# Kernel tuning notes

Measured on AMD Instinct MI355X. Metric: run time of the kernel, lower is better.

The kernel has to match this reference:

```python
import jax, jax.numpy as jnp
import numpy as np

EPS = 1e-8
N_ITERS = 5
B, L, K = 8192, 512, 4
EXP_SMOOTH = 0.99


def setup_inputs() -> dict:
    key = jax.random.key(0)
    k1, k2 = jax.random.split(key)
    windows = jax.random.normal(k1, (B, L), dtype=jnp.float32)
    noise = jax.random.normal(k2, (B, K), dtype=jnp.float32)  # replaces torch.randn_like
    init_centers = jnp.linspace(-0.75, 0.75, K, dtype=jnp.float32)
    init_scales = jnp.ones((K,), jnp.float32)
    init_weights = jnp.ones((K,), jnp.float32) / K
    prior_w_param = jnp.ones((1,), jnp.float32) * 10.0
    # log(exp_smooth ** arange(L-1, -1, -1)) reshaped to [L, 1]
    log_weights = (jnp.arange(L - 1, -1, -1, dtype=jnp.float32) * np.float32(np.log(EXP_SMOOTH))).reshape(L, 1)
    blend_param = jnp.ones((1,), jnp.float32) * 10.0
    return dict(windows=windows, noise=noise, init_centers=init_centers,
                init_scales=init_scales, init_weights=init_weights,
                prior_w_param=prior_w_param, log_weights=log_weights,
                blend_param=blend_param)


def _forward(windows, noise, init_centers, init_scales, init_weights,
             prior_w_param, log_weights, blend_param):
    # ---- _initialize_parameters ----
    data_mean = jnp.mean(windows, axis=-1, keepdims=True)        # [B,1]
    data_std = jnp.std(windows, axis=-1, ddof=1, keepdims=True)  # [B,1] (torch unbiased std)
    mu = init_centers[None, :] * data_std + data_mean            # [B,K]
    mu = mu + noise * data_std * 0.01                            # additive init noise
    sigma = jnp.abs(init_scales)[None, :] * data_std             # [B,K]
    w = jnp.broadcast_to(init_weights[None, :], mu.shape)        # [B,K]
    w, mu, sigma = w[:, None, :], mu[:, None, :], sigma[:, None, :]  # [B,1,K]

    # ---- _get_parameters ----
    weights = jnp.exp(log_weights)             # [L,1] exp-smoothing window weights
    blender = jax.nn.sigmoid(blend_param)      # [1]
    prior_w = jax.nn.sigmoid(prior_w_param)    # [1]

    x = windows[..., None]                     # [B,L,1]
    # NOTE: faithful to source — the loop never feeds (p,a,b) back into (w,mu,sigma),
    # so every iteration computes the identical E/M step.
    for _ in range(N_ITERS):
        # E-step: responsibilities via stable logsumexp over components
        log_mix = -0.5 * ((x - mu) / (sigma + EPS)) ** 2 + jnp.log((w + EPS) / (sigma + EPS))  # [B,L,K]
        g = jnp.exp(log_mix - jax.scipy.special.logsumexp(log_mix, axis=-1, keepdims=True))    # [B,L,K]
        # M-step
        wg = g * weights                                                  # [B,L,K]
        sum_g = jnp.maximum(jnp.sum(wg, axis=-2, keepdims=True), EPS)     # [B,1,K]
        p = sum_g + prior_w
        p = p / jnp.sum(p, axis=-1, keepdims=True)                        # mixture weights
        data_mu = jnp.sum(wg * x, axis=-2, keepdims=True) / sum_g         # [B,1,K]
        prior_mu = jnp.mean(x, axis=-2, keepdims=True)                    # [B,1,1] (broadcast ~ repeat)
        a = data_mu * blender + prior_mu * (1.0 - blender)                # blended means
        diff = x - a                                                      # [B,L,K]
        prior_var = jnp.var(x, axis=-2, ddof=1, keepdims=True)            # [B,1,1] unbiased
        data_var = jnp.sum(wg * diff ** 2, axis=-2, keepdims=True) / sum_g
        b = jnp.sqrt(data_var * blender + prior_var * (1.0 - blender) + EPS)  # blended stds
    return g, jnp.squeeze(p, -2), jnp.squeeze(a, -2), jnp.squeeze(b, -2)


def reference(windows, noise, init_centers, init_scales, init_weights,
              prior_w_param, log_weights, blend_param):
    return _forward(windows, noise, init_centers, init_scales, init_weights,
                    prior_w_param, log_weights, blend_param)
```

## Files before the change

### kernel.cpp

```cpp
#include <hip/hip_runtime.h>

#define EPS 1e-8f
constexpr int Bn = 8192, Ln = 512, Kn = 4;
constexpr int EPT = Ln / 64;

typedef float f32x4 __attribute__((ext_vector_type(4)));

__global__ __launch_bounds__(256, 4) void em_kernel(
    const float* __restrict__ windows,
    const float* __restrict__ noise,
    const float* __restrict__ init_centers,
    const float* __restrict__ init_scales,
    const float* __restrict__ init_weights,
    const float* __restrict__ prior_w_param,
    const float* __restrict__ log_weights,
    const float* __restrict__ blend_param,
    float* __restrict__ g_out,
    float* __restrict__ p_out,
    float* __restrict__ a_out,
    float* __restrict__ b_out)
{
    const int wave = threadIdx.x >> 6;
    const int lane = threadIdx.x & 63;
    const int gw   = blockIdx.x * 4 + wave;
    const int rowA = gw * 2;
    const int rowB = rowA + 1;

    float xA[EPT], xB[EPT], wl[EPT];
    const float* xrowA = windows + (size_t)rowA * Ln;
    const float* xrowB = windows + (size_t)rowB * Ln;
    #pragma unroll
    for (int j = 0; j < EPT; ++j) xA[j] = xrowA[lane + 64 * j];
    #pragma unroll
    for (int j = 0; j < EPT; ++j) xB[j] = xrowB[lane + 64 * j];
    #pragma unroll
    for (int j = 0; j < EPT; ++j) wl[j] = log_weights[lane + 64 * j];
    float nzA[Kn], nzB[Kn];
    #pragma unroll
    for (int k = 0; k < Kn; ++k) nzA[k] = noise[(size_t)rowA * Kn + k];
    #pragma unroll
    for (int k = 0; k < Kn; ++k) nzB[k] = noise[(size_t)rowB * Kn + k];

    const float pw = 1.0f / (1.0f + __expf(-prior_w_param[0]));
    const float bl = 1.0f / (1.0f + __expf(-blend_param[0]));

    #pragma unroll
    for (int j = 0; j < EPT; ++j) wl[j] = __expf(wl[j]);

    #pragma unroll
    for (int r = 0; r < 2; ++r) {
        const int    row = (r == 0) ? rowA : rowB;
        const float* x   = (r == 0) ? xA   : xB;
        const float* nz  = (r == 0) ? nzA  : nzB;

        float s = 0.f, sq = 0.f;
        #pragma unroll
        for (int j = 0; j < EPT; ++j) { s += x[j]; sq = fmaf(x[j], x[j], sq); }
        #pragma unroll
        for (int off = 32; off; off >>= 1) {
            s  += __shfl_xor(s,  off, 64);
            sq += __shfl_xor(sq, off, 64);
        }
        const float mean = s * (1.0f / (float)Ln);
        float var = (sq - s * s * (1.0f / (float)Ln)) * (1.0f / (float)(Ln - 1));
        var = fmaxf(var, 0.f);
        const float stdv = sqrtf(var);

        float mu[Kn], inv_sig[Kn], logc[Kn];
        #pragma unroll
        for (int k = 0; k < Kn; ++k) {
            float m  = fmaf(init_centers[k], stdv, mean) + nz[k] * stdv * 0.01f;
            float is = 1.0f / (fabsf(init_scales[k]) * stdv + EPS);
            mu[k]      = m;
            inv_sig[k] = is;
            logc[k]    = __logf((init_weights[k] + EPS) * is);
        }

        float s0[Kn] = {0,0,0,0}, s1[Kn] = {0,0,0,0}, s2[Kn] = {0,0,0,0};

        #pragma unroll
        for (int j = 0; j < EPT; ++j) {
            const int   l  = lane + 64 * j;
            const float xv = x[j];
            float lm[Kn];
            float mx = -1e30f;
            #pragma unroll
            for (int k = 0; k < Kn; ++k) {
                float t = (xv - mu[k]) * inv_sig[k];
                lm[k] = fmaf(t * t, -0.5f, logc[k]);
                mx = fmaxf(mx, lm[k]);
            }
            float e[Kn], sum = 0.f;
            #pragma unroll
            for (int k = 0; k < Kn; ++k) { e[k] = __expf(lm[k] - mx); sum += e[k]; }
            float inv = 1.0f / sum;
            f32x4 gv;
            gv.x = e[0] * inv; gv.y = e[1] * inv; gv.z = e[2] * inv; gv.w = e[3] * inv;
            reinterpret_cast<f32x4*>(g_out)[(size_t)row * Ln + l] = gv;

            float c   = wl[j] * inv;
            float xc  = xv * c;
            float x2c = xv * xc;
            #pragma unroll
            for (int k = 0; k < Kn; ++k) {
                s0[k] = fmaf(e[k], c,   s0[k]);
                s1[k] = fmaf(e[k], xc,  s1[k]);
                s2[k] = fmaf(e[k], x2c, s2[k]);
            }
        }

        #pragma unroll
        for (int k = 0; k < Kn; ++k) {
            #pragma unroll
            for (int off = 32; off; off >>= 1) {
                s0[k] += __shfl_xor(s0[k], off, 64);
                s1[k] += __shfl_xor(s1[k], off, 64);
                s2[k] += __shfl_xor(s2[k], off, 64);
            }
        }

        if (lane < Kn) {
            const int k = lane;
            float psum = 0.f;
            #pragma unroll
            for (int kk = 0; kk < Kn; ++kk) psum += fmaxf(s0[kk], EPS) + pw;
            float sg   = fmaxf(s0[k], EPS);
            float dmu  = s1[k] / sg;
            float av   = dmu * bl + mean * (1.0f - bl);
            float dvar = (s2[k] - 2.0f * av * s1[k] + av * av * s0[k]) / sg;
            float bv   = sqrtf(dvar * bl + var * (1.0f - bl) + EPS);
            p_out[(size_t)row * Kn + k] = (sg + pw) / psum;
            a_out[(size_t)row * Kn + k] = av;
            b_out[(size_t)row * Kn + k] = bv;
        }
    }
}

extern "C" void kernel_launch(void* const* d_in, const int* in_sizes, int n_in,
                              void* d_out, int out_size, void* d_ws, size_t ws_size,
                              hipStream_t stream) {
    const float* windows       = (const float*)d_in[0];
    const float* noise         = (const float*)d_in[1];
    const float* init_centers  = (const float*)d_in[2];
    const float* init_scales   = (const float*)d_in[3];
    const float* init_weights  = (const float*)d_in[4];
    const float* prior_w_param = (const float*)d_in[5];
    const float* log_weights   = (const float*)d_in[6];
    const float* blend_param   = (const float*)d_in[7];

    float* out = (float*)d_out;
    const size_t G  = (size_t)Bn * Ln * Kn;
    const size_t BK = (size_t)Bn * Kn;
    float* g_out = out;
    float* p_out = out + G;
    float* a_out = out + G + BK;
    float* b_out = out + G + 2 * BK;

    em_kernel<<<dim3(Bn / 8), dim3(256), 0, stream>>>(
        windows, noise, init_centers, init_scales, init_weights,
        prior_w_param, log_weights, blend_param,
        g_out, p_out, a_out, b_out);
}
```

Baseline: 24.28 us.

## Split EM into separate stats and streaming kernels using workspace

Splits the fused kernel into two kernels. A stats kernel computes per-row mean, variance and the initial component parameters and writes them to a workspace. A streaming kernel then reads those values, reloads the window rows and does the E/M pass with one row per wave instead of two. The aim is to shorten the serial dependency inside each wave and expose more parallelism, at the cost of a second kernel launch, a second read of the windows, and a workspace round-trip. The original fused kernel remains as a fallback when the workspace is too small.

```diff
diff --git a/kernel.cpp b/kernel.cpp
--- a/kernel.cpp
+++ b/kernel.cpp
@@ -3,10 +3,151 @@
 #define EPS 1e-8f
 constexpr int Bn = 8192, Ln = 512, Kn = 4;
 constexpr int EPT = Ln / 64;
+constexpr int WS_STRIDE = 16;
 
 typedef float f32x4 __attribute__((ext_vector_type(4)));
 
-__global__ __launch_bounds__(256, 4) void em_kernel(
+__global__ __launch_bounds__(256, 8) void stats_kernel(
+    const float* __restrict__ windows,
+    const float* __restrict__ noise,
+    const float* __restrict__ init_centers,
+    const float* __restrict__ init_scales,
+    const float* __restrict__ init_weights,
+    float* __restrict__ ws)
+{
+    const int wave = threadIdx.x >> 6;
+    const int lane = threadIdx.x & 63;
+    const int row  = blockIdx.x * 4 + wave;
+
+    const float* xr = windows + (size_t)row * Ln;
+    float x[EPT];
+    #pragma unroll
+    for (int j = 0; j < EPT; ++j) x[j] = xr[lane + 64 * j];
+
+    float s = 0.f, sq = 0.f;
+    #pragma unroll
+    for (int j = 0; j < EPT; ++j) { s += x[j]; sq = fmaf(x[j], x[j], sq); }
+    #pragma unroll
+    for (int off = 32; off; off >>= 1) {
+        s  += __shfl_xor(s,  off, 64);
+        sq += __shfl_xor(sq, off, 64);
+    }
+    const float mean = s * (1.0f / (float)Ln);
+    float var = (sq - s * s * (1.0f / (float)Ln)) * (1.0f / (float)(Ln - 1));
+    var = fmaxf(var, 0.f);
+    const float stdv = sqrtf(var);
+
+    if (lane < Kn) {
+        const int k  = lane;
+        float m  = fmaf(init_centers[k], stdv, mean) + noise[(size_t)row * Kn + k] * stdv * 0.01f;
+        float is = 1.0f / (fabsf(init_scales[k]) * stdv + EPS);
+        float lc = __logf((init_weights[k] + EPS) * is);
+        float* wr = ws + (size_t)row * WS_STRIDE;
+        wr[k]     = m;
+        wr[4 + k] = is;
+        wr[8 + k] = lc;
+        if (k == 0) { wr[12] = mean; wr[13] = var; }
+    }
+}
+
+__global__ __launch_bounds__(256, 4) void stream_kernel(
+    const float* __restrict__ windows,
+    const float* __restrict__ log_weights,
+    const float* __restrict__ prior_w_param,
+    const float* __restrict__ blend_param,
+    const float* __restrict__ ws,
+    float* __restrict__ g_out,
+    float* __restrict__ p_out,
+    float* __restrict__ a_out,
+    float* __restrict__ b_out)
+{
+    const int wave = threadIdx.x >> 6;
+    const int lane = threadIdx.x & 63;
+    const int row  = blockIdx.x * 4 + wave;
+
+    const float* wr = ws + (size_t)row * WS_STRIDE;
+    const f32x4 cmu = *reinterpret_cast<const f32x4*>(wr);
+    const f32x4 cis = *reinterpret_cast<const f32x4*>(wr + 4);
+    const f32x4 clc = *reinterpret_cast<const f32x4*>(wr + 8);
+    const f32x4 cmv = *reinterpret_cast<const f32x4*>(wr + 12);
+
+    const float* xr = windows + (size_t)row * Ln;
+    float x[EPT], wl[EPT];
+    #pragma unroll
+    for (int j = 0; j < EPT; ++j) x[j]  = xr[lane + 64 * j];
+    #pragma unroll
+    for (int j = 0; j < EPT; ++j) wl[j] = log_weights[lane + 64 * j];
+
+    const float pw = 1.0f / (1.0f + __expf(-prior_w_param[0]));
+    const float bl = 1.0f / (1.0f + __expf(-blend_param[0]));
+
+    #pragma unroll
+    for (int j = 0; j < EPT; ++j) wl[j] = __expf(wl[j]);
+
+    float mu[Kn]      = {cmu.x, cmu.y, cmu.z, cmu.w};
+    float inv_sig[Kn] = {cis.x, cis.y, cis.z, cis.w};
+    float logc[Kn]    = {clc.x, clc.y, clc.z, clc.w};
+    const float mean = cmv.x, var = cmv.y;
+
+    float s0[Kn] = {0,0,0,0}, s1[Kn] = {0,0,0,0}, s2[Kn] = {0,0,0,0};
+
+    #pragma unroll
+    for (int j = 0; j < EPT; ++j) {
+        const int   l  = lane + 64 * j;
+        const float xv = x[j];
+        float lm[Kn];
+        float mx = -1e30f;
+        #pragma unroll
+        for (int k = 0; k < Kn; ++k) {
+            float t = (xv - mu[k]) * inv_sig[k];
+            lm[k] = fmaf(t * t, -0.5f, logc[k]);
+            mx = fmaxf(mx, lm[k]);
+        }
+        float e[Kn], sum = 0.f;
+        #pragma unroll
+        for (int k = 0; k < Kn; ++k) { e[k] = __expf(lm[k] - mx); sum += e[k]; }
+        float inv = 1.0f / sum;
+        f32x4 gv;
+        gv.x = e[0] * inv; gv.y = e[1] * inv; gv.z = e[2] * inv; gv.w = e[3] * inv;
+        reinterpret_cast<f32x4*>(g_out)[(size_t)row * Ln + l] = gv;
+
+        float c   = wl[j] * inv;
+        float xc  = xv * c;
+        float x2c = xv * xc;
+        #pragma unroll
+        for (int k = 0; k < Kn; ++k) {
+            s0[k] = fmaf(e[k], c,   s0[k]);
+            s1[k] = fmaf(e[k], xc,  s1[k]);
+            s2[k] = fmaf(e[k], x2c, s2[k]);
+        }
+    }
+
+    #pragma unroll
+    for (int off = 32; off; off >>= 1)
+        #pragma unroll
+        for (int k = 0; k < Kn; ++k) {
+            s0[k] += __shfl_xor(s0[k], off, 64);
+            s1[k] += __shfl_xor(s1[k], off, 64);
+            s2[k] += __shfl_xor(s2[k], off, 64);
+        }
+
+    if (lane < Kn) {
+        const int k = lane;
+        float psum = 0.f;
+        #pragma unroll
+        for (int kk = 0; kk < Kn; ++kk) psum += fmaxf(s0[kk], EPS) + pw;
+        float sg   = fmaxf(s0[k], EPS);
+        float dmu  = s1[k] / sg;
+        float av   = dmu * bl + mean * (1.0f - bl);
+        float dvar = (s2[k] - 2.0f * av * s1[k] + av * av * s0[k]) / sg;
+        float bv   = sqrtf(dvar * bl + var * (1.0f - bl) + EPS);
+        p_out[(size_t)row * Kn + k] = (sg + pw) / psum;
+        a_out[(size_t)row * Kn + k] = av;
+        b_out[(size_t)row * Kn + k] = bv;
+    }
+}
+
+__global__ __launch_bounds__(256, 4) void em_kernel_fused(
     const float* __restrict__ windows,
     const float* __restrict__ noise,
     const float* __restrict__ init_centers,
@@ -77,7 +218,6 @@
         }
 
         float s0[Kn] = {0,0,0,0}, s1[Kn] = {0,0,0,0}, s2[Kn] = {0,0,0,0};
-
         #pragma unroll
         for (int j = 0; j < EPT; ++j) {
             const int   l  = lane + 64 * j;
@@ -110,14 +250,13 @@
         }
 
         #pragma unroll
-        for (int k = 0; k < Kn; ++k) {
-            #pragma unroll
-            for (int off = 32; off; off >>= 1) {
+        for (int off = 32; off; off >>= 1)
+            #pragma unroll
+            for (int k = 0; k < Kn; ++k) {
                 s0[k] += __shfl_xor(s0[k], off, 64);
                 s1[k] += __shfl_xor(s1[k], off, 64);
                 s2[k] += __shfl_xor(s2[k], off, 64);
             }
-        }
 
         if (lane < Kn) {
             const int k = lane;
@@ -156,8 +295,18 @@
     float* a_out = out + G + BK;
     float* b_out = out + G + 2 * BK;
 
-    em_kernel<<<dim3(Bn / 8), dim3(256), 0, stream>>>(
-        windows, noise, init_centers, init_scales, init_weights,
-        prior_w_param, log_weights, blend_param,
-        g_out, p_out, a_out, b_out);
+    const size_t ws_need = (size_t)Bn * WS_STRIDE * sizeof(float);
+    if (ws_size >= ws_need) {
+        float* ws = (float*)d_ws;
+        stats_kernel<<<dim3(Bn / 4), dim3(256), 0, stream>>>(
+            windows, noise, init_centers, init_scales, init_weights, ws);
+        stream_kernel<<<dim3(Bn / 4), dim3(256), 0, stream>>>(
+            windows, log_weights, prior_w_param, blend_param, ws,
+            g_out, p_out, a_out, b_out);
+    } else {
+        em_kernel_fused<<<dim3(Bn / 8), dim3(256), 0, stream>>>(
+            windows, noise, init_centers, init_scales, init_weights,
+            prior_w_param, log_weights, blend_param,
+            g_out, p_out, a_out, b_out);
+    }
 }
```

Result: slower. 25.95 us (+6.8%).
